# Performance work log

Hardware: AMD Instinct MI355X
Metric: run time of the kernel (lower is better)

Reference implementation:

```python
import jax, jax.numpy as jnp
import numpy as np

N, E, IN, HID, OUT, H = 50000, 400000, 128, 32, 64, 4
HID_DIM = HID * H  # 128


def _param(key, shape, scale=0.05):
    return jax.random.normal(key, shape, dtype=jnp.float32) * scale


def setup_inputs() -> dict:
    key = jax.random.key(0)
    ks = jax.random.split(key, 32)
    inp = {
        "x": jax.random.normal(ks[0], (N, IN), dtype=jnp.float32),
        "edge_index": jax.random.randint(ks[1], (2, E), 0, N, dtype=jnp.int32),
        "edge_weight": jax.random.uniform(ks[2], (E,), dtype=jnp.float32),
        # layer 0: in=128 -> H=4, C=32, concat => 128
        "Wl0": _param(ks[3], (IN, H * HID)), "bl0": jnp.zeros((H * HID,), jnp.float32),
        "Wr0": _param(ks[4], (IN, H * HID)), "br0": jnp.zeros((H * HID,), jnp.float32),
        "We0": _param(ks[5], (1, H * HID)),
        "att0": _param(ks[6], (H, HID)),
        "b0": jnp.zeros((H * HID,), jnp.float32),
        "g0": jnp.ones((H * HID,), jnp.float32), "be0": jnp.zeros((H * HID,), jnp.float32),
        # layer 1: in=128 -> H=4, C=64, concat=False (mean over heads) => 64
        "Wl1": _param(ks[7], (HID_DIM, H * OUT)), "bl1": jnp.zeros((H * OUT,), jnp.float32),
        "Wr1": _param(ks[8], (HID_DIM, H * OUT)), "br1": jnp.zeros((H * OUT,), jnp.float32),
        "We1": _param(ks[9], (1, H * OUT)),
        "att1": _param(ks[10], (H, OUT)),
        "b1": jnp.zeros((OUT,), jnp.float32),
        "g1": jnp.ones((OUT,), jnp.float32), "be1": jnp.zeros((OUT,), jnp.float32),
        # residual projections
        "P0": _param(ks[11], (IN, HID_DIM)), "pb0": jnp.zeros((HID_DIM,), jnp.float32),
        "P1": _param(ks[12], (HID_DIM, OUT)), "pb1": jnp.zeros((OUT,), jnp.float32),
    }
    return inp


def _add_self_loops(src, dst, ew):
    # PyG add_self_loops with fill_value='mean': loop attr = mean of incoming edge attrs per node
    s = jax.ops.segment_sum(ew, dst, num_segments=N)
    cnt = jax.ops.segment_sum(jnp.ones_like(ew), dst, num_segments=N)
    loop_w = s / jnp.maximum(cnt, 1.0)
    idx = jnp.arange(N, dtype=src.dtype)
    return jnp.concatenate([src, idx]), jnp.concatenate([dst, idx]), jnp.concatenate([ew, loop_w])


def _gatv2_layer(x, src, dst, ew, Wl, bl, Wr, br, We, att, b, g, be, C, concat):
    xl = (x @ Wl + bl).reshape(N, H, C)  # source transform (lin_l)
    xr = (x @ Wr + br).reshape(N, H, C)  # target transform (lin_r)
    eattr = (ew[:, None] @ We).reshape(-1, H, C)
    e = jax.nn.leaky_relu(xl[src] + xr[dst] + eattr, 0.2)  # [E', H, C]
    logits = jnp.einsum('ehc,hc->eh', e, att)
    # segment softmax over target nodes
    m = jax.ops.segment_max(logits, dst, num_segments=N)
    p = jnp.exp(logits - m[dst])
    denom = jax.ops.segment_sum(p, dst, num_segments=N)
    alpha = p / denom[dst]
    out = jax.ops.segment_sum(xl[src] * alpha[..., None], dst, num_segments=N)  # [N, H, C]
    if concat:
        out = out.reshape(N, H * C) + b
    else:
        out = out.mean(axis=1) + b
    out = jax.nn.elu(out)
    mu = out.mean(-1, keepdims=True)
    var = out.var(-1, keepdims=True)
    return (out - mu) / jnp.sqrt(var + 1e-5) * g + be


def reference(x, edge_index, edge_weight,
              Wl0, bl0, Wr0, br0, We0, att0, b0, g0, be0,
              Wl1, bl1, Wr1, br1, We1, att1, b1, g1, be1,
              P0, pb0, P1, pb1):
    src, dst, ew = _add_self_loops(edge_index[0], edge_index[1], edge_weight)
    h = x
    h1 = _gatv2_layer(h, src, dst, ew, Wl0, bl0, Wr0, br0, We0, att0, b0, g0, be0, HID, True)
    h = h1 + (h @ P0 + pb0)
    h2 = _gatv2_layer(h, src, dst, ew, Wl1, bl1, Wr1, br1, We1, att1, b1, g1, be1, OUT, False)
    h = h2 + (h @ P1 + pb1)
    return h
```

## Files before the change

kernel.cpp:

```cpp
#include <hip/hip_runtime.h>
#include <math.h>

#define N_NODES 50000
#define N_EDGES 400000
#define NPAD    50176
#define MROWS   50048
#define HC0 128
#define HC1 256
#define CSR_TOTAL (N_NODES + N_EDGES)

typedef short    bf16x8 __attribute__((ext_vector_type(8)));
typedef float    f32x4  __attribute__((ext_vector_type(4)));
typedef _Float16 h2     __attribute__((ext_vector_type(2)));
typedef _Float16 h4     __attribute__((ext_vector_type(4)));
typedef _Float16 h8     __attribute__((ext_vector_type(8)));

__device__ inline unsigned short f2bf(float f) {
  union { float f; unsigned u; } v; v.f = f;
  unsigned r = v.u + 0x7FFFu + ((v.u >> 16) & 1u);
  return (unsigned short)(r >> 16);
}
__device__ inline h2 mkh2(float a, float b) {
  h2 r; r[0] = (_Float16)a; r[1] = (_Float16)b; return r;
}
__device__ inline float hdot2(h2 a, h2 b, float c) {
#if __has_builtin(__builtin_amdgcn_fdot2)
  return __builtin_amdgcn_fdot2(a, b, c, false);
#else
  return c + (float)a[0] * (float)b[0] + (float)a[1] * (float)b[1];
#endif
}

__global__ void deg_kernel(const int* __restrict__ ei, const float* __restrict__ ew,
                           float* __restrict__ s, int* __restrict__ deg) {
  int e = blockIdx.x * 256 + threadIdx.x;
  if (e < N_EDGES) {
    int dst = ei[N_EDGES + e];
    atomicAdd(&s[dst], ew[e]);
    atomicAdd(&deg[dst], 1);
  }
}

__global__ void scan1(const int* __restrict__ deg, int* __restrict__ part,
                      int* __restrict__ bsum) {
  int i = blockIdx.x * 256 + threadIdx.x;
  int lane = threadIdx.x & 63, wid = threadIdx.x >> 6;
  int v = (i < N_NODES) ? deg[i] + 1 : 0;
  int inc = v;
#pragma unroll
  for (int d = 1; d < 64; d <<= 1) { int y = __shfl_up(inc, d, 64); if (lane >= d) inc += y; }
  __shared__ int wsum[4];
  if (lane == 63) wsum[wid] = inc;
  __syncthreads();
  int off = 0;
#pragma unroll
  for (int w = 0; w < 4; ++w) { int sv = wsum[w]; if (w < wid) off += sv; }
  part[i] = inc - v + off;
  if (threadIdx.x == 0) bsum[blockIdx.x] = wsum[0] + wsum[1] + wsum[2] + wsum[3];
}

__global__ void scan2(int* __restrict__ bsum) {
  int t = threadIdx.x;
  int lane = t & 63, wid = t >> 6;
  int v = (t < 196) ? bsum[t] : 0;
  int inc = v;
#pragma unroll
  for (int d = 1; d < 64; d <<= 1) { int y = __shfl_up(inc, d, 64); if (lane >= d) inc += y; }
  __shared__ int wsum[4];
  if (lane == 63) wsum[wid] = inc;
  __syncthreads();
  int off = 0;
#pragma unroll
  for (int w = 0; w < 4; ++w) { int sv = wsum[w]; if (w < wid) off += sv; }
  if (t < 196) bsum[t] = inc - v + off;
}

__global__ void self_kernel(const float* __restrict__ s, const int* __restrict__ deg,
                            const int* __restrict__ part, const int* __restrict__ bsum,
                            int2* __restrict__ csr2) {
  int i = blockIdx.x * 256 + threadIdx.x;
  if (i >= N_NODES) return;
  float w = s[i] / fmaxf((float)deg[i], 1.0f);
  int start = part[i] + bsum[i >> 8];
  csr2[start] = make_int2(i, __float_as_int(w));
}

__global__ void scatter_kernel(const int* __restrict__ ei, const float* __restrict__ ew,
                               const int* __restrict__ part, const int* __restrict__ bsum,
                               int* __restrict__ cursor, int2* __restrict__ csr2) {
  int e = blockIdx.x * 256 + threadIdx.x;
  if (e >= N_EDGES) return;
  int dst = ei[N_EDGES + e];
  int pos = atomicAdd(&cursor[dst], 1);
  int idx = part[dst] + bsum[dst >> 8] + 1 + pos;
  csr2[idx] = make_int2(ei[e], __float_as_int(ew[e]));
}

__global__ void pack_w(const float* __restrict__ Wl0, const float* __restrict__ Wr0,
                       const float* __restrict__ P0,  const float* __restrict__ Wl1,
                       const float* __restrict__ Wr1, const float* __restrict__ P1,
                       unsigned short* __restrict__ o_wl0, unsigned short* __restrict__ o_wr0,
                       unsigned short* __restrict__ o_p0,  unsigned short* __restrict__ o_wl1,
                       unsigned short* __restrict__ o_wr1, unsigned short* __restrict__ o_p1) {
  int n = blockIdx.x, k = threadIdx.x;
  const float* W; unsigned short* O; int N, nl;
  if      (n < 128) { W = Wl0; O = o_wl0; N = 128; nl = n; }
  else if (n < 256) { W = Wr0; O = o_wr0; N = 128; nl = n - 128; }
  else if (n < 384) { W = P0;  O = o_p0;  N = 128; nl = n - 256; }
  else if (n < 640) { W = Wl1; O = o_wl1; N = 256; nl = n - 384; }
  else if (n < 896) { W = Wr1; O = o_wr1; N = 256; nl = n - 640; }
  else              { W = P1;  O = o_p1;  N = 64;  nl = n - 896; }
  O[nl * 128 + k] = f2bf(W[(size_t)k * N + nl]);
}

__global__ __launch_bounds__(256) void gemm_l0(
    const float* __restrict__ X, const unsigned short* __restrict__ BT,
    const float* __restrict__ bias0, const float* __restrict__ bias1,
    const float* __restrict__ bias2,
    _Float16* __restrict__ o_xl, _Float16* __restrict__ o_xr,
    _Float16* __restrict__ o_h, int M) {
  __shared__ unsigned short As[64 * 136];
  const int tid = threadIdx.x;
  const int rbase = blockIdx.x * 64;
#pragma unroll
  for (int i = 0; i < 8; ++i) {
    int c = i * 256 + tid;
    int row = c >> 5, c4 = c & 31;
    int ar = rbase + row; if (ar > M - 1) ar = M - 1;
    float4 v = *(const float4*)(X + (size_t)ar * 128 + c4 * 4);
    ushort4 o; o.x = f2bf(v.x); o.y = f2bf(v.y); o.z = f2bf(v.z); o.w = f2bf(v.w);
    *(ushort4*)(As + row * 136 + c4 * 4) = o;
  }
  __syncthreads();
  const int w = tid >> 6, l = tid & 63;
  const int lr = l & 15, lg = l >> 4;
#pragma unroll
  for (int i = 0; i < 6; ++i) {
    const int ct = w * 6 + i;
    const bf16x8* bp = (const bf16x8*)(BT + (size_t)(ct * 16 + lr) * 128 + lg * 8);
    bf16x8 b0 = bp[0], b1 = bp[4], b2 = bp[8], b3 = bp[12];
    const int colb = ct * 16 + lg * 4;
    const int cc = colb & 127;
    const float* bptr = (ct < 8 ? bias0 : (ct < 16 ? bias1 : bias2));
    float4 bv = *(const float4*)(bptr + cc);
#pragma unroll
    for (int rt = 0; rt < 4; ++rt) {
      const unsigned short* ap = As + (rt * 16 + lr) * 136 + lg * 8;
      bf16x8 a0 = *(const bf16x8*)(ap);
      bf16x8 a1 = *(const bf16x8*)(ap + 32);
      bf16x8 a2 = *(const bf16x8*)(ap + 64);
      bf16x8 a3 = *(const bf16x8*)(ap + 96);
      f32x4 acc = {0.f, 0.f, 0.f, 0.f};
      acc = __builtin_amdgcn_mfma_f32_16x16x32_bf16(b0, a0, acc, 0, 0, 0);
      acc = __builtin_amdgcn_mfma_f32_16x16x32_bf16(b1, a1, acc, 0, 0, 0);
      acc = __builtin_amdgcn_mfma_f32_16x16x32_bf16(b2, a2, acc, 0, 0, 0);
      acc = __builtin_amdgcn_mfma_f32_16x16x32_bf16(b3, a3, acc, 0, 0, 0);
      const int row = rbase + rt * 16 + lr;
      h4 o;
      o[0] = (_Float16)(acc[0] + bv.x); o[1] = (_Float16)(acc[1] + bv.y);
      o[2] = (_Float16)(acc[2] + bv.z); o[3] = (_Float16)(acc[3] + bv.w);
      _Float16* dst = (ct < 8) ? o_xl : (ct < 16 ? o_xr : o_h);
      *(h4*)(dst + (size_t)row * 128 + cc) = o;
    }
  }
}

__global__ __launch_bounds__(256) void gemm_l1(
    const unsigned short* __restrict__ A, const unsigned short* __restrict__ BT,
    const float* __restrict__ bias0, const float* __restrict__ bias1,
    const float* __restrict__ bias2,
    _Float16* __restrict__ o_xl, _Float16* __restrict__ o_xr,
    float* __restrict__ o_out, int M) {
  __shared__ unsigned short As[64 * 136];
  const int tid = threadIdx.x;
  const int rbase = blockIdx.x * 64;
#pragma unroll
  for (int i = 0; i < 4; ++i) {
    int c = i * 256 + tid;
    int row = c >> 4, slot = c & 15;
    int ar = rbase + row; if (ar > M - 1) ar = M - 1;
    uint4 v = *(const uint4*)(A + (size_t)ar * 128 + slot * 8);
    *(uint4*)(As + row * 136 + slot * 8) = v;
  }
  __syncthreads();
  const int w = tid >> 6, l = tid & 63;
  const int lr = l & 15, lg = l >> 4;
#pragma unroll
  for (int i = 0; i < 9; ++i) {
    const int ct = w * 9 + i;
    const bf16x8* bp = (const bf16x8*)(BT + (size_t)(ct * 16 + lr) * 128 + lg * 8);
    bf16x8 b0 = bp[0], b1 = bp[4], b2 = bp[8], b3 = bp[12];
    const int colb = ct * 16 + lg * 4;
    const int cc = (ct < 32) ? (colb & 255) : (colb - 512);
    const float* bptr = (ct < 16 ? bias0 : (ct < 32 ? bias1 : bias2));
    float4 bv = *(const float4*)(bptr + cc);
#pragma unroll
    for (int rt = 0; rt < 4; ++rt) {
      const unsigned short* ap = As + (rt * 16 + lr) * 136 + lg * 8;
      bf16x8 a0 = *(const bf16x8*)(ap);
      bf16x8 a1 = *(const bf16x8*)(ap + 32);
      bf16x8 a2 = *(const bf16x8*)(ap + 64);
      bf16x8 a3 = *(const bf16x8*)(ap + 96);
      f32x4 acc = {0.f, 0.f, 0.f, 0.f};
      acc = __builtin_amdgcn_mfma_f32_16x16x32_bf16(b0, a0, acc, 0, 0, 0);
      acc = __builtin_amdgcn_mfma_f32_16x16x32_bf16(b1, a1, acc, 0, 0, 0);
      acc = __builtin_amdgcn_mfma_f32_16x16x32_bf16(b2, a2, acc, 0, 0, 0);
      acc = __builtin_amdgcn_mfma_f32_16x16x32_bf16(b3, a3, acc, 0, 0, 0);
      const int row = rbase + rt * 16 + lr;
      if (ct < 32) {
        h4 o;
        o[0] = (_Float16)(acc[0] + bv.x); o[1] = (_Float16)(acc[1] + bv.y);
        o[2] = (_Float16)(acc[2] + bv.z); o[3] = (_Float16)(acc[3] + bv.w);
        *(h4*)((ct < 16 ? o_xl : o_xr) + (size_t)row * 256 + cc) = o;
      } else if (row < M) {
        float4 o;
        o.x = acc[0] + bv.x; o.y = acc[1] + bv.y;
        o.z = acc[2] + bv.z; o.w = acc[3] + bv.w;
        *(float4*)(o_out + (size_t)row * 64 + cc) = o;
      }
    }
  }
}

__device__ inline void edge_step0(int2 rec, h8 a8, bool valid,
                                  const h2* xrv2, const h2* wef2, const h2* att2,
                                  h2* acc2, float& den) {
  _Float16 wh = (_Float16)__int_as_float(rec.y);
  h2 w2; w2[0] = wh; w2[1] = wh;
  const h2 c02 = mkh2(0.2f, 0.2f);
  int4 ai = __builtin_bit_cast(int4, a8);
  h2 av[4];
  av[0] = __builtin_bit_cast(h2, ai.x); av[1] = __builtin_bit_cast(h2, ai.y);
  av[2] = __builtin_bit_cast(h2, ai.z); av[3] = __builtin_bit_cast(h2, ai.w);
  float c = 0.f;
#pragma unroll
  for (int k = 0; k < 4; ++k) {
    h2 sv = av[k] + (w2 * wef2[k] + xrv2[k]);
    h2 lk = __builtin_elementwise_max(sv, sv * c02);
    c = hdot2(lk, att2[k], c);
  }
  c += __shfl_xor(c, 1, 64); c += __shfl_xor(c, 2, 64);
  float p = valid ? __expf(c) : 0.f;
  den += p;
  _Float16 ph = (_Float16)p;
  h2 p2; p2[0] = ph; p2[1] = ph;
#pragma unroll
  for (int k = 0; k < 4; ++k) acc2[k] = p2 * av[k] + acc2[k];
}

__device__ inline void edge_step1(int2 rec, h8 a8, bool valid,
                                  const h2* xrv2, const h2* wef2, const h2* att2,
                                  h2* acc2, float& den) {
  _Float16 wh = (_Float16)__int_as_float(rec.y);
  h2 w2; w2[0] = wh; w2[1] = wh;
  const h2 c02 = mkh2(0.2f, 0.2f);
  int4 ai = __builtin_bit_cast(int4, a8);
  h2 av[4];
  av[0] = __builtin_bit_cast(h2, ai.x); av[1] = __builtin_bit_cast(h2, ai.y);
  av[2] = __builtin_bit_cast(h2, ai.z); av[3] = __builtin_bit_cast(h2, ai.w);
  float c = 0.f;
#pragma unroll
  for (int k = 0; k < 4; ++k) {
    h2 sv = av[k] + (w2 * wef2[k] + xrv2[k]);
    h2 lk = __builtin_elementwise_max(sv, sv * c02);
    c = hdot2(lk, att2[k], c);
  }
  c += __shfl_xor(c, 1, 64); c += __shfl_xor(c, 2, 64); c += __shfl_xor(c, 4, 64);
  float p = valid ? __expf(c) : 0.f;
  den += p;
  _Float16 ph = (_Float16)p;
  h2 p2; p2[0] = ph; p2[1] = ph;
#pragma unroll
  for (int k = 0; k < 4; ++k) acc2[k] = p2 * av[k] + acc2[k];
}

__global__ __launch_bounds__(64) void agg0(
    const int* __restrict__ part, const int* __restrict__ bsum,
    const int* __restrict__ deg, const int2* __restrict__ csr2,
    const _Float16* __restrict__ xl, const _Float16* __restrict__ xr,
    const float* __restrict__ We, const float* __restrict__ att,
    const float* __restrict__ b, const float* __restrict__ g,
    const float* __restrict__ be, const _Float16* __restrict__ hres,
    unsigned short* __restrict__ hout) {
  const int l = threadIdx.x & 63;
  const int n = blockIdx.x;
  const int grp = l >> 4, cl = l & 15, c0 = cl * 8;
  h2 xrv2[4], wef2[4], att2[4];
  {
    h8 x8 = *(const h8*)(xr + (size_t)n * HC0 + c0);
    int4 xi = __builtin_bit_cast(int4, x8);
    xrv2[0] = __builtin_bit_cast(h2, xi.x); xrv2[1] = __builtin_bit_cast(h2, xi.y);
    xrv2[2] = __builtin_bit_cast(h2, xi.z); xrv2[3] = __builtin_bit_cast(h2, xi.w);
    float4 w0 = *(const float4*)(We + c0),  w1 = *(const float4*)(We + c0 + 4);
    float4 t0 = *(const float4*)(att + c0), t1 = *(const float4*)(att + c0 + 4);
    wef2[0] = mkh2(w0.x, w0.y); wef2[1] = mkh2(w0.z, w0.w);
    wef2[2] = mkh2(w1.x, w1.y); wef2[3] = mkh2(w1.z, w1.w);
    att2[0] = mkh2(t0.x, t0.y); att2[1] = mkh2(t0.z, t0.w);
    att2[2] = mkh2(t1.x, t1.y); att2[3] = mkh2(t1.z, t1.w);
  }
  const int start = part[n] + bsum[n >> 8];
  const int cnt   = deg[n] + 1;
  const int2* seg = csr2 + start;
  h2 acc2[4] = {};
  float den = 0.f;
  int2 rA0 = seg[grp],      rA1 = seg[grp + 4];
  int2 rB0 = seg[grp + 8],  rB1 = seg[grp + 12];
  h8 aA0 = *(const h8*)(xl + (size_t)rA0.x * HC0 + c0);
  h8 aA1 = *(const h8*)(xl + (size_t)rA1.x * HC0 + c0);
  const int trips = (cnt + 7) >> 3;
  int e = grp;
  for (int t = 0; t < trips; ++t) {
    int2 rC0 = seg[e + 16], rC1 = seg[e + 20];
    h8 aB0 = *(const h8*)(xl + (size_t)rB0.x * HC0 + c0);
    h8 aB1 = *(const h8*)(xl + (size_t)rB1.x * HC0 + c0);
    edge_step0(rA0, aA0, e < cnt,     xrv2, wef2, att2, acc2, den);
    edge_step0(rA1, aA1, e + 4 < cnt, xrv2, wef2, att2, acc2, den);
    rA0 = rB0; rA1 = rB1; rB0 = rC0; rB1 = rC1; aA0 = aB0; aA1 = aB1;
    e += 8;
  }
  den += __shfl_xor(den, 16, 64); den += __shfl_xor(den, 32, 64);
#pragma unroll
  for (int k = 0; k < 4; ++k) {
    int b16 = __shfl_xor(__builtin_bit_cast(int, acc2[k]), 16, 64);
    acc2[k] = acc2[k] + __builtin_bit_cast(h2, b16);
    int b32 = __shfl_xor(__builtin_bit_cast(int, acc2[k]), 32, 64);
    acc2[k] = acc2[k] + __builtin_bit_cast(h2, b32);
  }
  float v[8], s1 = 0.f, s2 = 0.f;
  float dinv = 1.f / den;
  {
    float4 b0v = *(const float4*)(b + c0), b1v = *(const float4*)(b + c0 + 4);
    float bb[8] = {b0v.x,b0v.y,b0v.z,b0v.w,b1v.x,b1v.y,b1v.z,b1v.w};
#pragma unroll
    for (int j = 0; j < 8; ++j) {
      float t = (float)acc2[j >> 1][j & 1] * dinv + bb[j];
      t = t > 0.f ? t : __expf(t) - 1.f;
      v[j] = t; s1 += t; s2 += t * t;
    }
  }
  s1 += __shfl_xor(s1, 1, 64); s2 += __shfl_xor(s2, 1, 64);
  s1 += __shfl_xor(s1, 2, 64); s2 += __shfl_xor(s2, 2, 64);
  s1 += __shfl_xor(s1, 4, 64); s2 += __shfl_xor(s2, 4, 64);
  s1 += __shfl_xor(s1, 8, 64); s2 += __shfl_xor(s2, 8, 64);
  float mean = s1 * (1.f / 128.f);
  float inv  = rsqrtf(s2 * (1.f / 128.f) - mean * mean + 1e-5f);
  if (grp == 0) {
    float4 g0v = *(const float4*)(g + c0),  g1v = *(const float4*)(g + c0 + 4);
    float4 e0v = *(const float4*)(be + c0), e1v = *(const float4*)(be + c0 + 4);
    h8 hh = *(const h8*)(hres + (size_t)n * HC0 + c0);
    float gg[8] = {g0v.x,g0v.y,g0v.z,g0v.w,g1v.x,g1v.y,g1v.z,g1v.w};
    float ee[8] = {e0v.x,e0v.y,e0v.z,e0v.w,e1v.x,e1v.y,e1v.z,e1v.w};
    bf16x8 o;
#pragma unroll
    for (int j = 0; j < 8; ++j)
      o[j] = (short)f2bf((v[j] - mean) * inv * gg[j] + ee[j] + (float)hh[j]);
    *(bf16x8*)(hout + (size_t)n * HC0 + c0) = o;
  }
}

__global__ __launch_bounds__(64) void agg1(
    const int* __restrict__ part, const int* __restrict__ bsum,
    const int* __restrict__ deg, const int2* __restrict__ csr2,
    const _Float16* __restrict__ xl, const _Float16* __restrict__ xr,
    const float* __restrict__ We, const float* __restrict__ att,
    const float* __restrict__ b, const float* __restrict__ g,
    const float* __restrict__ be, float* __restrict__ out) {
  const int l = threadIdx.x & 63;
  const int n = blockIdx.x;
  const int grp = l >> 5, cl = l & 31, c0 = cl * 8;
  h2 xrv2[4], wef2[4], att2[4];
  {
    h8 x8 = *(const h8*)(xr + (size_t)n * HC1 + c0);
    int4 xi = __builtin_bit_cast(int4, x8);
    xrv2[0] = __builtin_bit_cast(h2, xi.x); xrv2[1] = __builtin_bit_cast(h2, xi.y);
    xrv2[2] = __builtin_bit_cast(h2, xi.z); xrv2[3] = __builtin_bit_cast(h2, xi.w);
    float4 w0 = *(const float4*)(We + c0),  w1 = *(const float4*)(We + c0 + 4);
    float4 t0 = *(const float4*)(att + c0), t1 = *(const float4*)(att + c0 + 4);
    wef2[0] = mkh2(w0.x, w0.y); wef2[1] = mkh2(w0.z, w0.w);
    wef2[2] = mkh2(w1.x, w1.y); wef2[3] = mkh2(w1.z, w1.w);
    att2[0] = mkh2(t0.x, t0.y); att2[1] = mkh2(t0.z, t0.w);
    att2[2] = mkh2(t1.x, t1.y); att2[3] = mkh2(t1.z, t1.w);
  }
  const int start = part[n] + bsum[n >> 8];
  const int cnt   = deg[n] + 1;
  const int2* seg = csr2 + start;
  h2 acc2[4] = {};
  float den = 0.f;
  int2 rA0 = seg[grp],     rA1 = seg[grp + 2];
  int2 rB0 = seg[grp + 4], rB1 = seg[grp + 6];
  h8 aA0 = *(const h8*)(xl + (size_t)rA0.x * HC1 + c0);
  h8 aA1 = *(const h8*)(xl + (size_t)rA1.x * HC1 + c0);
  const int trips = (cnt + 3) >> 2;
  int e = grp;
  for (int t = 0; t < trips; ++t) {
    int2 rC0 = seg[e + 8], rC1 = seg[e + 10];
    h8 aB0 = *(const h8*)(xl + (size_t)rB0.x * HC1 + c0);
    h8 aB1 = *(const h8*)(xl + (size_t)rB1.x * HC1 + c0);
    edge_step1(rA0, aA0, e < cnt,     xrv2, wef2, att2, acc2, den);
    edge_step1(rA1, aA1, e + 2 < cnt, xrv2, wef2, att2, acc2, den);
    rA0 = rB0; rA1 = rB1; rB0 = rC0; rB1 = rC1; aA0 = aB0; aA1 = aB1;
    e += 4;
  }
  den += __shfl_xor(den, 32, 64);
#pragma unroll
  for (int k = 0; k < 4; ++k) {
    int b32 = __shfl_xor(__builtin_bit_cast(int, acc2[k]), 32, 64);
    acc2[k] = acc2[k] + __builtin_bit_cast(h2, b32);
  }
  float dinv = 1.f / den;
  float v[8], s1 = 0.f, s2 = 0.f;
  const int oc = (cl & 7) * 8;
  {
    float4 b0v = *(const float4*)(b + oc), b1v = *(const float4*)(b + oc + 4);
    float bb[8] = {b0v.x,b0v.y,b0v.z,b0v.w,b1v.x,b1v.y,b1v.z,b1v.w};
#pragma unroll
    for (int j = 0; j < 8; ++j) {
      float t = (float)acc2[j >> 1][j & 1] * dinv;
      t += __shfl_xor(t, 8, 64);
      t += __shfl_xor(t, 16, 64);
      t = t * 0.25f + bb[j];
      t = t > 0.f ? t : __expf(t) - 1.f;
      v[j] = t; s1 += t; s2 += t * t;
    }
  }
  s1 += __shfl_xor(s1, 1, 64); s2 += __shfl_xor(s2, 1, 64);
  s1 += __shfl_xor(s1, 2, 64); s2 += __shfl_xor(s2, 2, 64);
  s1 += __shfl_xor(s1, 4, 64); s2 += __shfl_xor(s2, 4, 64);
  float mean = s1 * (1.f / 64.f);
  float inv  = rsqrtf(s2 * (1.f / 64.f) - mean * mean + 1e-5f);
  if (grp == 0 && cl < 8) {
    float4 g0v = *(const float4*)(g + oc),  g1v = *(const float4*)(g + oc + 4);
    float4 e0v = *(const float4*)(be + oc), e1v = *(const float4*)(be + oc + 4);
    float gg[8] = {g0v.x,g0v.y,g0v.z,g0v.w,g1v.x,g1v.y,g1v.z,g1v.w};
    float ee[8] = {e0v.x,e0v.y,e0v.z,e0v.w,e1v.x,e1v.y,e1v.z,e1v.w};
    float* po = out + (size_t)n * 64 + oc;
    float4 o0 = *(const float4*)po, o1 = *(const float4*)(po + 4);
    o0.x += (v[0] - mean) * inv * gg[0] + ee[0];
    o0.y += (v[1] - mean) * inv * gg[1] + ee[1];
    o0.z += (v[2] - mean) * inv * gg[2] + ee[2];
    o0.w += (v[3] - mean) * inv * gg[3] + ee[3];
    o1.x += (v[4] - mean) * inv * gg[4] + ee[4];
    o1.y += (v[5] - mean) * inv * gg[5] + ee[5];
    o1.z += (v[6] - mean) * inv * gg[6] + ee[6];
    o1.w += (v[7] - mean) * inv * gg[7] + ee[7];
    *(float4*)po = o0; *(float4*)(po + 4) = o1;
  }
}

extern "C" void kernel_launch(void* const* d_in, const int* in_sizes, int n_in,
                              void* d_out, int out_size, void* d_ws, size_t ws_size,
                              hipStream_t stream) {
  const float* x    = (const float*)d_in[0];
  const int*   ei   = (const int*)  d_in[1];
  const float* ew   = (const float*)d_in[2];
  const float* Wl0  = (const float*)d_in[3];
  const float* bl0  = (const float*)d_in[4];
  const float* Wr0  = (const float*)d_in[5];
  const float* br0  = (const float*)d_in[6];
  const float* We0  = (const float*)d_in[7];
  const float* att0 = (const float*)d_in[8];
  const float* b0   = (const float*)d_in[9];
  const float* g0   = (const float*)d_in[10];
  const float* be0  = (const float*)d_in[11];
  const float* Wl1  = (const float*)d_in[12];
  const float* bl1  = (const float*)d_in[13];
  const float* Wr1  = (const float*)d_in[14];
  const float* br1  = (const float*)d_in[15];
  const float* We1  = (const float*)d_in[16];
  const float* att1 = (const float*)d_in[17];
  const float* b1   = (const float*)d_in[18];
  const float* g1   = (const float*)d_in[19];
  const float* be1  = (const float*)d_in[20];
  const float* P0   = (const float*)d_in[21];
  const float* pb0  = (const float*)d_in[22];
  const float* P1   = (const float*)d_in[23];
  const float* pb1  = (const float*)d_in[24];
  float* out = (float*)d_out;

  float* f        = (float*)d_ws;
  float* s_loopw  = f;
  int*   deg      = (int*)(f + 50176);
  int*   cursor   = (int*)(f + 100352);
  int*   part     = (int*)(f + 150528);
  int*   bsum     = (int*)(f + 200704);
  int2*  csr2     = (int2*)(f + 200960);
  unsigned short* wl0T = (unsigned short*)(f + 1102080);
  unsigned short* wr0T = wl0T + 16384;
  unsigned short* p0T  = wl0T + 32768;
  unsigned short* wl1T = (unsigned short*)(f + 1126656);
  unsigned short* wr1T = wl1T + 32768;
  unsigned short* p1T  = wl1T + 65536;
  unsigned short* hb   = (unsigned short*)(f + 1163520);
  _Float16*       hres = (_Float16*)(f + 4366592);
  _Float16*       RA   = (_Float16*)(f + 7569664);
  _Float16*       RB   = (_Float16*)(f + 13975808);
  _Float16* xl0h = RA, *xr0h = RB;
  _Float16* xl1h = RA, *xr1h = RB;

  hipMemsetAsync(s_loopw, 0, (size_t)(50176 * 3) * sizeof(float), stream);
  hipMemsetAsync(csr2 + CSR_TOTAL, 0, 64 * sizeof(int2), stream);
  deg_kernel<<<(N_EDGES + 255) / 256, 256, 0, stream>>>(ei, ew, s_loopw, deg);
  scan1<<<NPAD / 256, 256, 0, stream>>>(deg, part, bsum);
  scan2<<<1, 256, 0, stream>>>(bsum);
  self_kernel<<<(N_NODES + 255) / 256, 256, 0, stream>>>(s_loopw, deg, part, bsum, csr2);
  scatter_kernel<<<(N_EDGES + 255) / 256, 256, 0, stream>>>(ei, ew, part, bsum,
                                                            cursor, csr2);

  pack_w<<<960, 128, 0, stream>>>(Wl0, Wr0, P0, Wl1, Wr1, P1,
                                  wl0T, wr0T, p0T, wl1T, wr1T, p1T);

  const int GB = MROWS / 64;
  gemm_l0<<<GB, 256, 0, stream>>>(x, wl0T, bl0, br0, pb0, xl0h, xr0h, hres, N_NODES);
  agg0<<<N_NODES, 64, 0, stream>>>(part, bsum, deg, csr2,
                                   xl0h, xr0h, We0, att0, b0, g0, be0, hres, hb);

  gemm_l1<<<GB, 256, 0, stream>>>(hb, wl1T, bl1, br1, pb1, xl1h, xr1h, out, N_NODES);
  agg1<<<N_NODES, 64, 0, stream>>>(part, bsum, deg, csr2,
                                   xl1h, xr1h, We1, att1, b1, g1, be1, out);
}
```

Before: 219.5 us.

## Fuse CSR build and weight packing into one launch; swizzle aggregation node order

Merges the self-loop fill, the edge scatter, the weight transpose/bf16 pack and the csr padding memset into a single kernel whose block ranges select the role. This removes several launches and serial gaps. Separately, the two aggregation kernels remap block IDs so consecutive blocks visit nodes spread across eight strided chunks, which changes locality and load balance across the XCDs. The remap may help or hurt cache reuse of the CSR and feature rows.

```diff
diff --git a/kernel.cpp b/kernel.cpp
--- a/kernel.cpp
+++ b/kernel.cpp
@@ -8,6 +8,9 @@
 #define HC0 128
 #define HC1 256
 #define CSR_TOTAL (N_NODES + N_EDGES)
+#define EB 1563
+#define NB 196
+#define PB 480
 
 typedef short    bf16x8 __attribute__((ext_vector_type(8)));
 typedef float    f32x4  __attribute__((ext_vector_type(4)));
@@ -75,42 +78,45 @@
   if (t < 196) bsum[t] = inc - v + off;
 }
 
-__global__ void self_kernel(const float* __restrict__ s, const int* __restrict__ deg,
+__global__ void fused_build(const int* __restrict__ ei, const float* __restrict__ ew,
+                            const float* __restrict__ s, const int* __restrict__ deg,
                             const int* __restrict__ part, const int* __restrict__ bsum,
-                            int2* __restrict__ csr2) {
-  int i = blockIdx.x * 256 + threadIdx.x;
-  if (i >= N_NODES) return;
-  float w = s[i] / fmaxf((float)deg[i], 1.0f);
-  int start = part[i] + bsum[i >> 8];
-  csr2[start] = make_int2(i, __float_as_int(w));
-}
-
-__global__ void scatter_kernel(const int* __restrict__ ei, const float* __restrict__ ew,
-                               const int* __restrict__ part, const int* __restrict__ bsum,
-                               int* __restrict__ cursor, int2* __restrict__ csr2) {
-  int e = blockIdx.x * 256 + threadIdx.x;
-  if (e >= N_EDGES) return;
-  int dst = ei[N_EDGES + e];
-  int pos = atomicAdd(&cursor[dst], 1);
-  int idx = part[dst] + bsum[dst >> 8] + 1 + pos;
-  csr2[idx] = make_int2(ei[e], __float_as_int(ew[e]));
-}
-
-__global__ void pack_w(const float* __restrict__ Wl0, const float* __restrict__ Wr0,
-                       const float* __restrict__ P0,  const float* __restrict__ Wl1,
-                       const float* __restrict__ Wr1, const float* __restrict__ P1,
-                       unsigned short* __restrict__ o_wl0, unsigned short* __restrict__ o_wr0,
-                       unsigned short* __restrict__ o_p0,  unsigned short* __restrict__ o_wl1,
-                       unsigned short* __restrict__ o_wr1, unsigned short* __restrict__ o_p1) {
-  int n = blockIdx.x, k = threadIdx.x;
-  const float* W; unsigned short* O; int N, nl;
-  if      (n < 128) { W = Wl0; O = o_wl0; N = 128; nl = n; }
-  else if (n < 256) { W = Wr0; O = o_wr0; N = 128; nl = n - 128; }
-  else if (n < 384) { W = P0;  O = o_p0;  N = 128; nl = n - 256; }
-  else if (n < 640) { W = Wl1; O = o_wl1; N = 256; nl = n - 384; }
-  else if (n < 896) { W = Wr1; O = o_wr1; N = 256; nl = n - 640; }
-  else              { W = P1;  O = o_p1;  N = 64;  nl = n - 896; }
-  O[nl * 128 + k] = f2bf(W[(size_t)k * N + nl]);
+                            int* __restrict__ cursor, int2* __restrict__ csr2,
+                            const float* __restrict__ Wl0, const float* __restrict__ Wr0,
+                            const float* __restrict__ P0,  const float* __restrict__ Wl1,
+                            const float* __restrict__ Wr1, const float* __restrict__ P1,
+                            unsigned short* __restrict__ o_wl0, unsigned short* __restrict__ o_wr0,
+                            unsigned short* __restrict__ o_p0,  unsigned short* __restrict__ o_wl1,
+                            unsigned short* __restrict__ o_wr1, unsigned short* __restrict__ o_p1) {
+  const int bid = blockIdx.x;
+  if (bid < EB) {
+    int e = bid * 256 + threadIdx.x;
+    if (e >= N_EDGES) return;
+    int dst = ei[N_EDGES + e];
+    int pos = atomicAdd(&cursor[dst], 1);
+    int idx = part[dst] + bsum[dst >> 8] + 1 + pos;
+    csr2[idx] = make_int2(ei[e], __float_as_int(ew[e]));
+  } else if (bid < EB + NB) {
+    int i = (bid - EB) * 256 + threadIdx.x;
+    if (i < N_NODES) {
+      float w = s[i] / fmaxf((float)deg[i], 1.0f);
+      int start = part[i] + bsum[i >> 8];
+      csr2[start] = make_int2(i, __float_as_int(w));
+    } else if (i - N_NODES < 64) {
+      csr2[CSR_TOTAL + (i - N_NODES)] = make_int2(0, 0);
+    }
+  } else {
+    int n = (bid - EB - NB) * 2 + (threadIdx.x >> 7);
+    int k = threadIdx.x & 127;
+    const float* W; unsigned short* O; int N, nl;
+    if      (n < 128) { W = Wl0; O = o_wl0; N = 128; nl = n; }
+    else if (n < 256) { W = Wr0; O = o_wr0; N = 128; nl = n - 128; }
+    else if (n < 384) { W = P0;  O = o_p0;  N = 128; nl = n - 256; }
+    else if (n < 640) { W = Wl1; O = o_wl1; N = 256; nl = n - 384; }
+    else if (n < 896) { W = Wr1; O = o_wr1; N = 256; nl = n - 640; }
+    else              { W = P1;  O = o_p1;  N = 64;  nl = n - 896; }
+    O[nl * 128 + k] = f2bf(W[(size_t)k * N + nl]);
+  }
 }
 
 __global__ __launch_bounds__(256) void gemm_l0(
@@ -283,7 +289,8 @@
     const float* __restrict__ be, const _Float16* __restrict__ hres,
     unsigned short* __restrict__ hout) {
   const int l = threadIdx.x & 63;
-  const int n = blockIdx.x;
+  const int bid = blockIdx.x;
+  const int n = (bid & 7) * (N_NODES / 8) + (bid >> 3);
   const int grp = l >> 4, cl = l & 15, c0 = cl * 8;
   h2 xrv2[4], wef2[4], att2[4];
   {
@@ -366,7 +373,8 @@
     const float* __restrict__ b, const float* __restrict__ g,
     const float* __restrict__ be, float* __restrict__ out) {
   const int l = threadIdx.x & 63;
-  const int n = blockIdx.x;
+  const int bid = blockIdx.x;
+  const int n = (bid & 7) * (N_NODES / 8) + (bid >> 3);
   const int grp = l >> 5, cl = l & 31, c0 = cl * 8;
   h2 xrv2[4], wef2[4], att2[4];
   {
@@ -498,16 +506,13 @@
   _Float16* xl1h = RA, *xr1h = RB;
 
   hipMemsetAsync(s_loopw, 0, (size_t)(50176 * 3) * sizeof(float), stream);
-  hipMemsetAsync(csr2 + CSR_TOTAL, 0, 64 * sizeof(int2), stream);
   deg_kernel<<<(N_EDGES + 255) / 256, 256, 0, stream>>>(ei, ew, s_loopw, deg);
   scan1<<<NPAD / 256, 256, 0, stream>>>(deg, part, bsum);
   scan2<<<1, 256, 0, stream>>>(bsum);
-  self_kernel<<<(N_NODES + 255) / 256, 256, 0, stream>>>(s_loopw, deg, part, bsum, csr2);
-  scatter_kernel<<<(N_EDGES + 255) / 256, 256, 0, stream>>>(ei, ew, part, bsum,
-                                                            cursor, csr2);
-
-  pack_w<<<960, 128, 0, stream>>>(Wl0, Wr0, P0, Wl1, Wr1, P1,
-                                  wl0T, wr0T, p0T, wl1T, wr1T, p1T);
+  fused_build<<<EB + NB + PB, 256, 0, stream>>>(ei, ew, s_loopw, deg, part, bsum,
+                                                cursor, csr2,
+                                                Wl0, Wr0, P0, Wl1, Wr1, P1,
+                                                wl0T, wr0T, p0T, wl1T, wr1T, p1T);
 
   const int GB = MROWS / 64;
   gemm_l0<<<GB, 256, 0, stream>>>(x, wl0T, bl0, br0, pb0, xl0h, xr0h, hres, N_NODES);
```

New measurement: 210.2 us, median of 2. -4.2%, faster.
